# Performance work log

Hardware: AMD Instinct MI355X
Metric: run time of the kernel (lower is better)

## Reference

```python
import jax, jax.numpy as jnp
import numpy as np

D_MODEL = 1024
NUM_HEADS = 16
D_HEAD = D_MODEL // NUM_HEADS
EPS = 1e-06


def setup_inputs() -> dict:
    key = jax.random.key(0)
    ks = jax.random.split(key, 11)
    B, T = 16, 8192
    s = 1.0 / np.sqrt(D_MODEL)
    inp = {
        "query": jax.random.normal(ks[0], (B, 1, D_MODEL), jnp.float32),
        "key": jax.random.normal(ks[1], (B, T, D_MODEL), jnp.float32),
        "value": jax.random.normal(ks[2], (B, T, D_MODEL), jnp.float32),
        "Wq": jax.random.normal(ks[3], (D_MODEL, D_MODEL), jnp.float32) * s,
        "bq": jnp.zeros((D_MODEL,), jnp.float32),
        "Wk": jax.random.normal(ks[4], (D_MODEL, D_MODEL), jnp.float32) * s,
        "bk": jnp.zeros((D_MODEL,), jnp.float32),
        "Wv": jax.random.normal(ks[5], (D_MODEL, D_MODEL), jnp.float32) * s,
        "bv": jnp.zeros((D_MODEL,), jnp.float32),
        "Wo": jax.random.normal(ks[6], (D_MODEL, D_MODEL), jnp.float32) * s,
        "bo": jnp.zeros((D_MODEL,), jnp.float32),
    }
    return inp


def _feature_map(x):
    # ELU + 1 ensures positivity
    return jax.nn.elu(x) + 1.0


def reference(query, key, value, Wq, bq, Wk, bk, Wv, bv, Wo, bo):
    B, T, _ = key.shape
    H, dh = NUM_HEADS, D_HEAD
    # projections (torch Linear: x @ W^T + b)
    Q = (query @ Wq.T + bq).reshape(B, 1, H, dh).transpose(0, 2, 1, 3)  # [B,H,1,dh]
    K = (key @ Wk.T + bk).reshape(B, T, H, dh).transpose(0, 2, 1, 3)    # [B,H,T,dh]
    V = (value @ Wv.T + bv).reshape(B, T, H, dh).transpose(0, 2, 1, 3)  # [B,H,T,dh]
    Q = _feature_map(Q)
    K = _feature_map(K)
    # linear-attention accumulators
    KV = jnp.einsum("bhtd,bhte->bhde", K, V)        # [B,H,dh,dh]
    Z = K.sum(axis=2)                                  # [B,H,dh]
    num = jnp.einsum("bhqd,bhde->bhqe", Q, KV)       # [B,H,1,dh]
    den = jnp.einsum("bhqd,bhd->bhq", Q, Z)[..., None]  # [B,H,1,1]
    out = num / (den + EPS)
    out = out.transpose(0, 2, 1, 3).reshape(B, 1, D_MODEL)
    return out @ Wo.T + bo
```

## Files before the change

kernel.cpp:

```cpp
#include <hip/hip_runtime.h>


typedef __attribute__((ext_vector_type(8))) short  bf16x8;
typedef __attribute__((ext_vector_type(4))) short  bf16x4;
typedef __attribute__((ext_vector_type(4))) float  f32x4;

#define WS_QPHI  0u
#define WS_PRE   65536u
#define WS_S     131072u
#define WS_WKB   1179648u
#define WS_W     3276800u
#define WS_SPART 11665408u
#define WS_NEED  (11665408u + 33554432u)

__device__ __forceinline__ unsigned short f2bf(float f) {
  union { float f; unsigned u; } c; c.f = f;
  unsigned u = c.u;
  return (unsigned short)((u + 0x7fffu + ((u >> 16) & 1u)) >> 16);
}

__device__ __forceinline__ unsigned cvt_pk_bf16(float lo, float hi) {
  unsigned r;
  asm("v_cvt_pk_bf16_f32 %0, %1, %2" : "=v"(r) : "v"(lo), "v"(hi));
  return r;
}

__device__ __forceinline__ uint4 pack_bf16x8(f32x4 x, f32x4 y) {
  uint4 r;
  r.x = cvt_pk_bf16(x[0], x[1]); r.y = cvt_pk_bf16(x[2], x[3]);
  r.z = cvt_pk_bf16(y[0], y[1]); r.w = cvt_pk_bf16(y[2], y[3]);
  return r;
}

__device__ __forceinline__ void gload_lds16(const void* g, void* l) {
  __builtin_amdgcn_global_load_lds((const __attribute__((address_space(1))) void*)g,
                                   (__attribute__((address_space(3))) void*)l, 16, 0, 0);
}

__global__ __launch_bounds__(256)
void k_prep(const float* __restrict__ Wk, unsigned short* __restrict__ Wkb,
            const float* __restrict__ q, const float* __restrict__ Wq,
            const float* __restrict__ bq, float* __restrict__ Qphi) {
  __shared__ float red[4][64];
  const int tid = threadIdx.x;
  if (blockIdx.x < 1024) {
    int i = blockIdx.x * 256 + tid;
    f32x4 v = ((const f32x4*)Wk)[i];
    bf16x4 o;
    o[0] = (short)f2bf(v[0]); o[1] = (short)f2bf(v[1]);
    o[2] = (short)f2bf(v[2]); o[3] = (short)f2bf(v[3]);
    ((bf16x4*)Wkb)[i] = o;
    return;
  }
  const int lin = blockIdx.x - 1024;
  const int h = lin & 15, b = lin >> 4;
  const int d = tid & 63, part = tid >> 6;
  const f32x4* qr = (const f32x4*)(q + b * 1024) + part * 64;
  const f32x4* wr = (const f32x4*)(Wq + (size_t)(h * 64 + d) * 1024) + part * 64;
  float s = 0.f;
  #pragma unroll 8
  for (int i = 0; i < 64; ++i) {
    f32x4 a = qr[i], ww = wr[i];
    s += a[0]*ww[0] + a[1]*ww[1] + a[2]*ww[2] + a[3]*ww[3];
  }
  red[part][d] = s;
  __syncthreads();
  if (part == 0) {
    float t = red[0][d] + red[1][d] + red[2][d] + red[3][d] + bq[h * 64 + d];
    t = t > 0.f ? t + 1.f : __expf(t);
    Qphi[(b * 16 + h) * 64 + d] = t;
  }
}

__global__ __launch_bounds__(512, 4)
void k_kproj(const float* __restrict__ key, const unsigned short* __restrict__ Wkb,
             const float* __restrict__ bk, const float* __restrict__ Qphi,
             float* __restrict__ w) {
  __shared__ __align__(16) unsigned short sA[2][128 * 32];
  __shared__ __align__(16) unsigned short sB[4][256 * 32];

  const int bid  = blockIdx.x + (blockIdx.y << 2);
  const int work = ((bid & 7) << 9) | (bid >> 3);
  const int np   = work & 3;
  const int mb   = work >> 2;
  const int b    = mb >> 6;
  const int mrow = (mb & 63) << 7;
  const int tid  = threadIdx.x;
  const int lane = tid & 63;
  const int wv   = tid >> 6;
  const int wr   = wv >> 2;
  const int wc   = wv & 3;
  const int n0   = np << 8;
  const int h    = (np << 2) | wc;
  const int l15  = lane & 15;
  const int l16  = lane >> 4;

  const int lkx = ((l16 ^ ((l15 >> 1) & 3)) << 3);

  const int ra = tid >> 2, aq = tid & 3;
  const float* Ab = key + ((size_t)((b << 13) + mrow + ra)) * 1024 + aq * 8;
  const int sAoff = ra * 32 + ((aq ^ ((ra >> 1) & 3)) << 3);

  const int bsw = ((lane & 3) ^ ((lane >> 3) & 3)) << 3;
  const unsigned short* Bb = Wkb + ((size_t)(n0 + (wv << 5) + (lane >> 2))) * 1024 + bsw;

  f32x4 acc[4][4];
  #pragma unroll
  for (int i = 0; i < 4; ++i)
    #pragma unroll
    for (int j = 0; j < 4; ++j) acc[i][j] = (f32x4)0.f;

  float qreg[4];
  #pragma unroll
  for (int ni = 0; ni < 4; ++ni)
    qreg[ni] = Qphi[((b << 4) + h) * 64 + ni * 16 + l15];

  f32x4 a0 = *(const f32x4*)(Ab);
  f32x4 a1 = *(const f32x4*)(Ab + 4);
  __builtin_amdgcn_sched_barrier(0);
  gload_lds16(Bb,                  &sB[0][wv * 1024]);
  gload_lds16(Bb + 16 * 1024,      &sB[0][wv * 1024 + 512]);
  gload_lds16(Bb + 32,             &sB[1][wv * 1024]);
  gload_lds16(Bb + 16 * 1024 + 32, &sB[1][wv * 1024 + 512]);
  gload_lds16(Bb + 64,             &sB[2][wv * 1024]);
  gload_lds16(Bb + 16 * 1024 + 64, &sB[2][wv * 1024 + 512]);
  __builtin_amdgcn_sched_barrier(0);
  *(uint4*)&sA[0][sAoff] = pack_bf16x8(a0, a1);
  asm volatile("s_waitcnt vmcnt(2) lgkmcnt(0)" ::: "memory");
  __builtin_amdgcn_s_barrier();
  __builtin_amdgcn_sched_barrier(0);

  bf16x8 bfr[4];
  #pragma unroll
  for (int ni = 0; ni < 4; ++ni)
    bfr[ni] = *(const bf16x8*)&sB[0][((wc << 6) + ni * 16 + l15) * 32 + lkx];

  #pragma unroll 1
  for (int t = 0; t < 32; ++t) {
    if (t < 31) {
      const float* An = Ab + (t + 1) * 32;
      a0 = *(const f32x4*)(An);
      a1 = *(const f32x4*)(An + 4);
    }
    __builtin_amdgcn_sched_barrier(0);
    if (t < 29) {
      const unsigned short* Bn = Bb + (t + 3) * 32;
      const int bn = (t + 3) & 3;
      gload_lds16(Bn,             &sB[bn][wv * 1024]);
      gload_lds16(Bn + 16 * 1024, &sB[bn][wv * 1024 + 512]);
    }
    __builtin_amdgcn_sched_barrier(0);
    {
      const unsigned short* pA = &sA[t & 1][0];
      bf16x8 af[4];
      #pragma unroll
      for (int mi = 0; mi < 4; ++mi)
        af[mi] = *(const bf16x8*)&pA[((wr << 6) + mi * 16 + l15) * 32 + lkx];
      #pragma unroll
      for (int mi = 0; mi < 4; ++mi)
        #pragma unroll
        for (int ni = 0; ni < 4; ++ni)
          acc[mi][ni] = __builtin_amdgcn_mfma_f32_16x16x32_bf16(af[mi], bfr[ni], acc[mi][ni], 0, 0, 0);
    }
    if (t < 31) {
      const unsigned short* pBn = &sB[(t + 1) & 3][0];
      #pragma unroll
      for (int ni = 0; ni < 4; ++ni)
        bfr[ni] = *(const bf16x8*)&pBn[((wc << 6) + ni * 16 + l15) * 32 + lkx];
    }
    if (t < 31)
      *(uint4*)&sA[(t + 1) & 1][sAoff] = pack_bf16x8(a0, a1);
    if (t <= 28)      asm volatile("s_waitcnt vmcnt(2) lgkmcnt(0)" ::: "memory");
    else if (t == 29) asm volatile("s_waitcnt vmcnt(0) lgkmcnt(0)" ::: "memory");
    else if (t == 30) asm volatile("s_waitcnt lgkmcnt(0)" ::: "memory");
    if (t < 31) {
      __builtin_amdgcn_s_barrier();
      __builtin_amdgcn_sched_barrier(0);
    }
  }

  float bias[4];
  #pragma unroll
  for (int ni = 0; ni < 4; ++ni) bias[ni] = bk[n0 + (wc << 6) + ni * 16 + l15];

  #pragma unroll
  for (int mi = 0; mi < 4; ++mi) {
    float wa[4];
    #pragma unroll
    for (int r = 0; r < 4; ++r) {
      float s = 0.f;
      #pragma unroll
      for (int ni = 0; ni < 4; ++ni) {
        float x = acc[mi][ni][r] + bias[ni];
        x = x > 0.f ? x + 1.f : __expf(x);
        s += x * qreg[ni];
      }
      wa[r] = s;
    }
    #pragma unroll
    for (int m = 1; m < 16; m <<= 1)
      #pragma unroll
      for (int r = 0; r < 4; ++r) wa[r] += __shfl_xor(wa[r], m, 64);
    if (l15 == 0) {
      #pragma unroll
      for (int r = 0; r < 4; ++r) {
        int trow = mrow + (wr << 6) + mi * 16 + (l16 << 2) + r;
        w[(((size_t)((b << 4) + h)) << 13) + trow] = wa[r];
      }
    }
  }
}

__global__ __launch_bounds__(256)
void k_sgemm_p(const float* __restrict__ value, const float* __restrict__ w,
               float* __restrict__ Spart) {
  __shared__ float wl[16 * 256];
  const int b = blockIdx.x, tc = blockIdx.y;
  const int t0 = tc << 8;
  const int tid = threadIdx.x;
  for (int i = tid; i < 16 * 256; i += 256)
    wl[i] = w[(((size_t)(b * 16 + (i >> 8))) << 13) + t0 + (i & 255)];
  __syncthreads();
  f32x4 acc[16];
  #pragma unroll
  for (int h = 0; h < 16; ++h) acc[h] = (f32x4)0.f;
  const f32x4* vb  = (const f32x4*)(value + ((size_t)(b << 13) + t0) * 1024) + tid;
  const f32x4* wl4 = (const f32x4*)wl;
  #pragma unroll 1
  for (int tq = 0; tq < 64; ++tq) {
    f32x4 x0 = vb[((tq << 2) + 0) << 8];
    f32x4 x1 = vb[((tq << 2) + 1) << 8];
    f32x4 x2 = vb[((tq << 2) + 2) << 8];
    f32x4 x3 = vb[((tq << 2) + 3) << 8];
    #pragma unroll
    for (int h = 0; h < 16; ++h) {
      f32x4 wv = wl4[(h << 6) + tq];
      acc[h] += x0 * wv[0];
      acc[h] += x1 * wv[1];
      acc[h] += x2 * wv[2];
      acc[h] += x3 * wv[3];
    }
  }
  #pragma unroll
  for (int h = 0; h < 16; ++h) {
    f32x4* op = (f32x4*)(Spart + (((size_t)((b * 32 + tc) * 16 + h)) << 10));
    op[tid] = acc[h];
  }
}

__global__ __launch_bounds__(256)
void k_numden_p(const float* __restrict__ w, const float* __restrict__ Spart,
                const float* __restrict__ Wv, const float* __restrict__ bv,
                float* __restrict__ pre) {
  __shared__ float red[2][4][64];
  const int b = blockIdx.x, h = blockIdx.y;
  const int tid = threadIdx.x, e = tid & 63, part = tid >> 6;
  const float* wb = w + (((size_t)(b * 16 + h)) << 13);
  float dsum = 0.f;
  for (int i = part * 32; i < part * 32 + 32; ++i) dsum += wb[i * 64 + e];
  const f32x4* sp  = (const f32x4*)(Spart + (((size_t)(b * 32 * 16 + h)) << 10));
  const f32x4* wvr = (const f32x4*)(Wv + (size_t)(h * 64 + e) * 1024);
  float ns = 0.f;
  for (int i = part * 64; i < part * 64 + 64; ++i) {
    f32x4 a = (f32x4)0.f;
    #pragma unroll 8
    for (int p = 0; p < 32; ++p) a += sp[p * 4096 + i];
    f32x4 c = wvr[i];
    ns += a[0]*c[0] + a[1]*c[1] + a[2]*c[2] + a[3]*c[3];
  }
  red[0][part][e] = dsum; red[1][part][e] = ns;
  __syncthreads();
  if (part == 0) {
    float d = red[0][0][e] + red[0][1][e] + red[0][2][e] + red[0][3][e];
    float n = red[1][0][e] + red[1][1][e] + red[1][2][e] + red[1][3][e];
    #pragma unroll
    for (int m = 1; m < 64; m <<= 1) d += __shfl_xor(d, m, 64);
    n += d * bv[h * 64 + e];
    pre[b * 1024 + h * 64 + e] = n / (d + 1e-6f);
  }
}

__global__ __launch_bounds__(256)
void k_sgemm(const float* __restrict__ value, const float* __restrict__ w,
             float* __restrict__ S) {
  __shared__ float wl[16 * 256];
  const int b = blockIdx.x, tc = blockIdx.y;
  const int t0 = tc << 8;
  const int tid = threadIdx.x;
  for (int i = tid; i < 16 * 256; i += 256)
    wl[i] = w[(((size_t)(b * 16 + (i >> 8))) << 13) + t0 + (i & 255)];
  __syncthreads();
  f32x4 acc[16];
  #pragma unroll
  for (int h = 0; h < 16; ++h) acc[h] = (f32x4)0.f;
  const f32x4* vb  = (const f32x4*)(value + ((size_t)(b << 13) + t0) * 1024) + tid;
  const f32x4* wl4 = (const f32x4*)wl;
  #pragma unroll 1
  for (int tq = 0; tq < 64; ++tq) {
    f32x4 x0 = vb[((tq << 2) + 0) << 8];
    f32x4 x1 = vb[((tq << 2) + 1) << 8];
    f32x4 x2 = vb[((tq << 2) + 2) << 8];
    f32x4 x3 = vb[((tq << 2) + 3) << 8];
    #pragma unroll
    for (int h = 0; h < 16; ++h) {
      f32x4 wv = wl4[(h << 6) + tq];
      acc[h] += x0 * wv[0]; acc[h] += x1 * wv[1];
      acc[h] += x2 * wv[2]; acc[h] += x3 * wv[3];
    }
  }
  #pragma unroll
  for (int h = 0; h < 16; ++h) {
    float* sp = S + ((b << 4) + h) * 1024 + (tid << 2);
    atomicAdd(sp + 0, acc[h][0]); atomicAdd(sp + 1, acc[h][1]);
    atomicAdd(sp + 2, acc[h][2]); atomicAdd(sp + 3, acc[h][3]);
  }
}

__global__ __launch_bounds__(256)
void k_numden(const float* __restrict__ w, const float* __restrict__ S,
              const float* __restrict__ Wv, const float* __restrict__ bv,
              float* __restrict__ pre) {
  __shared__ float red[2][4][64];
  const int b = blockIdx.x, h = blockIdx.y;
  const int tid = threadIdx.x, e = tid & 63, part = tid >> 6;
  const float* wb = w + (((size_t)(b * 16 + h)) << 13);
  float dsum = 0.f;
  for (int i = part * 32; i < part * 32 + 32; ++i) dsum += wb[i * 64 + e];
  const f32x4* sr  = (const f32x4*)(S + (b * 16 + h) * 1024);
  const f32x4* wvr = (const f32x4*)(Wv + (size_t)(h * 64 + e) * 1024);
  float ns = 0.f;
  for (int i = part * 64; i < part * 64 + 64; ++i) {
    f32x4 a = sr[i], c = wvr[i];
    ns += a[0]*c[0] + a[1]*c[1] + a[2]*c[2] + a[3]*c[3];
  }
  red[0][part][e] = dsum; red[1][part][e] = ns;
  __syncthreads();
  if (part == 0) {
    float d = red[0][0][e] + red[0][1][e] + red[0][2][e] + red[0][3][e];
    float n = red[1][0][e] + red[1][1][e] + red[1][2][e] + red[1][3][e];
    #pragma unroll
    for (int m = 1; m < 64; m <<= 1) d += __shfl_xor(d, m, 64);
    n += d * bv[h * 64 + e];
    pre[b * 1024 + h * 64 + e] = n / (d + 1e-6f);
  }
}

__global__ __launch_bounds__(256)
void k_outproj(const float* __restrict__ pre, const float* __restrict__ Wo,
               const float* __restrict__ bo, float* __restrict__ out) {
  __shared__ float pl[1024];
  const int lin = blockIdx.x;
  const int ch = lin & 7, b = lin >> 3;
  const int tid = threadIdx.x, lane = tid & 63, wv = tid >> 6;
  for (int i = tid; i < 1024; i += 256) pl[i] = pre[b * 1024 + i];
  __syncthreads();
  for (int oi = 0; oi < 32; ++oi) {
    int o = (ch << 7) + (wv << 5) + oi;
    const f32x4* wrow = (const f32x4*)(Wo + (size_t)o * 1024);
    float s = 0.f;
    #pragma unroll
    for (int j = 0; j < 4; ++j) {
      f32x4 v = wrow[lane * 4 + j];
      f32x4 p = *(const f32x4*)&pl[(lane * 4 + j) * 4];
      s += v[0]*p[0] + v[1]*p[1] + v[2]*p[2] + v[3]*p[3];
    }
    #pragma unroll
    for (int m = 1; m < 64; m <<= 1) s += __shfl_xor(s, m, 64);
    if (lane == 0) out[b * 1024 + o] = s + bo[o];
  }
}

extern "C" void kernel_launch(void* const* d_in, const int* in_sizes, int n_in,
                              void* d_out, int out_size, void* d_ws, size_t ws_size,
                              hipStream_t stream) {
  const float* query = (const float*)d_in[0];
  const float* key   = (const float*)d_in[1];
  const float* value = (const float*)d_in[2];
  const float* Wq    = (const float*)d_in[3];
  const float* bq    = (const float*)d_in[4];
  const float* Wk    = (const float*)d_in[5];
  const float* bk    = (const float*)d_in[6];
  const float* Wv    = (const float*)d_in[7];
  const float* bv    = (const float*)d_in[8];
  const float* Wo    = (const float*)d_in[9];
  const float* bo    = (const float*)d_in[10];
  float* out = (float*)d_out;
  char* ws = (char*)d_ws;
  float*          Qphi  = (float*)(ws + WS_QPHI);
  float*          pre   = (float*)(ws + WS_PRE);
  float*          S     = (float*)(ws + WS_S);
  unsigned short* Wkb   = (unsigned short*)(ws + WS_WKB);
  float*          w     = (float*)(ws + WS_W);
  float*          Spart = (float*)(ws + WS_SPART);

  k_prep<<<1280, 256, 0, stream>>>(Wk, Wkb, query, Wq, bq, Qphi);
  k_kproj<<<dim3(4, 1024), 512, 0, stream>>>(key, Wkb, bk, Qphi, w);
  if (ws_size >= (size_t)WS_NEED) {
    k_sgemm_p<<<dim3(16, 32), 256, 0, stream>>>(value, w, Spart);
    k_numden_p<<<dim3(16, 16), 256, 0, stream>>>(w, Spart, Wv, bv, pre);
  } else {
    hipMemsetAsync(S, 0, 16 * 16 * 1024 * sizeof(float), stream);
    k_sgemm<<<dim3(16, 32), 256, 0, stream>>>(value, w, S);
    k_numden<<<dim3(16, 16), 256, 0, stream>>>(w, S, Wv, bv, pre);
  }
  k_outproj<<<128, 256, 0, stream>>>(pre, Wo, bo, out);
}
```

Baseline: 589.1 us.

## Enlarge K-projection GEMM tile to 256 rows per block with 8x4 MFMA per wave

The key-projection GEMM block tile doubles from 128 to 256 rows of keys. Each wave now holds 8x4 accumulators instead of 4x4, and the grid is halved to 2048 blocks. Each Wk tile loaded into LDS is now reused across twice as many rows, cutting B traffic and LDS loads per MFMA. In exchange, accumulator registers and LDS per block go up, launch bounds drop to 2 blocks per CU, and the B-fragment register prefetch across iterations is removed.

```diff
diff --git a/kernel.cpp b/kernel.cpp
--- a/kernel.cpp
+++ b/kernel.cpp
@@ -72,19 +72,19 @@
   }
 }
 
-__global__ __launch_bounds__(512, 4)
+__global__ __launch_bounds__(512, 2)
 void k_kproj(const float* __restrict__ key, const unsigned short* __restrict__ Wkb,
              const float* __restrict__ bk, const float* __restrict__ Qphi,
              float* __restrict__ w) {
-  __shared__ __align__(16) unsigned short sA[2][128 * 32];
+  __shared__ __align__(16) unsigned short sA[2][256 * 32];
   __shared__ __align__(16) unsigned short sB[4][256 * 32];
 
-  const int bid  = blockIdx.x + (blockIdx.y << 2);
-  const int work = ((bid & 7) << 9) | (bid >> 3);
+  const int bid  = blockIdx.x;
+  const int work = ((bid & 7) << 8) | (bid >> 3);
   const int np   = work & 3;
   const int mb   = work >> 2;
-  const int b    = mb >> 6;
-  const int mrow = (mb & 63) << 7;
+  const int b    = mb >> 5;
+  const int mrow = (mb & 31) << 8;
   const int tid  = threadIdx.x;
   const int lane = tid & 63;
   const int wv   = tid >> 6;
@@ -97,16 +97,20 @@
 
   const int lkx = ((l16 ^ ((l15 >> 1) & 3)) << 3);
 
-  const int ra = tid >> 2, aq = tid & 3;
-  const float* Ab = key + ((size_t)((b << 13) + mrow + ra)) * 1024 + aq * 8;
-  const int sAoff = ra * 32 + ((aq ^ ((ra >> 1) & 3)) << 3);
+  const int ar  = tid >> 1;
+  const int ac0 = (tid & 1) << 1;
+  const int aS  = (ar >> 1) & 3;
+  const float* Ab = key + ((size_t)((b << 13) + mrow + ar)) * 1024 + ((tid & 1) << 4);
+  const int aw0 = ar * 32 + ((ac0 ^ aS) << 3);
+  const int aw1 = ar * 32 + (((ac0 | 1) ^ aS) << 3);
 
   const int bsw = ((lane & 3) ^ ((lane >> 3) & 3)) << 3;
-  const unsigned short* Bb = Wkb + ((size_t)(n0 + (wv << 5) + (lane >> 2))) * 1024 + bsw;
-
-  f32x4 acc[4][4];
-  #pragma unroll
-  for (int i = 0; i < 4; ++i)
+  const unsigned short* Bg0 = Wkb + ((size_t)(n0 + (wv << 4) + (lane >> 2))) * 1024 + bsw;
+  const unsigned short* Bg1 = Bg0 + 128 * 1024;
+
+  f32x4 acc[8][4];
+  #pragma unroll
+  for (int i = 0; i < 8; ++i)
     #pragma unroll
     for (int j = 0; j < 4; ++j) acc[i][j] = (f32x4)0.f;
 
@@ -117,23 +121,21 @@
 
   f32x4 a0 = *(const f32x4*)(Ab);
   f32x4 a1 = *(const f32x4*)(Ab + 4);
+  f32x4 a2 = *(const f32x4*)(Ab + 8);
+  f32x4 a3 = *(const f32x4*)(Ab + 12);
   __builtin_amdgcn_sched_barrier(0);
-  gload_lds16(Bb,                  &sB[0][wv * 1024]);
-  gload_lds16(Bb + 16 * 1024,      &sB[0][wv * 1024 + 512]);
-  gload_lds16(Bb + 32,             &sB[1][wv * 1024]);
-  gload_lds16(Bb + 16 * 1024 + 32, &sB[1][wv * 1024 + 512]);
-  gload_lds16(Bb + 64,             &sB[2][wv * 1024]);
-  gload_lds16(Bb + 16 * 1024 + 64, &sB[2][wv * 1024 + 512]);
+  gload_lds16(Bg0,      &sB[0][wv * 512]);
+  gload_lds16(Bg1,      &sB[0][4096 + wv * 512]);
+  gload_lds16(Bg0 + 32, &sB[1][wv * 512]);
+  gload_lds16(Bg1 + 32, &sB[1][4096 + wv * 512]);
+  gload_lds16(Bg0 + 64, &sB[2][wv * 512]);
+  gload_lds16(Bg1 + 64, &sB[2][4096 + wv * 512]);
   __builtin_amdgcn_sched_barrier(0);
-  *(uint4*)&sA[0][sAoff] = pack_bf16x8(a0, a1);
-  asm volatile("s_waitcnt vmcnt(2) lgkmcnt(0)" ::: "memory");
+  *(uint4*)&sA[0][aw0] = pack_bf16x8(a0, a1);
+  *(uint4*)&sA[0][aw1] = pack_bf16x8(a2, a3);
+  asm volatile("s_waitcnt vmcnt(4) lgkmcnt(0)" ::: "memory");
   __builtin_amdgcn_s_barrier();
   __builtin_amdgcn_sched_barrier(0);
-
-  bf16x8 bfr[4];
-  #pragma unroll
-  for (int ni = 0; ni < 4; ++ni)
-    bfr[ni] = *(const bf16x8*)&sB[0][((wc << 6) + ni * 16 + l15) * 32 + lkx];
 
   #pragma unroll 1
   for (int t = 0; t < 32; ++t) {
@@ -141,35 +143,36 @@
       const float* An = Ab + (t + 1) * 32;
       a0 = *(const f32x4*)(An);
       a1 = *(const f32x4*)(An + 4);
+      a2 = *(const f32x4*)(An + 8);
+      a3 = *(const f32x4*)(An + 12);
     }
     __builtin_amdgcn_sched_barrier(0);
     if (t < 29) {
-      const unsigned short* Bn = Bb + (t + 3) * 32;
       const int bn = (t + 3) & 3;
-      gload_lds16(Bn,             &sB[bn][wv * 1024]);
-      gload_lds16(Bn + 16 * 1024, &sB[bn][wv * 1024 + 512]);
+      gload_lds16(Bg0 + (t + 3) * 32, &sB[bn][wv * 512]);
+      gload_lds16(Bg1 + (t + 3) * 32, &sB[bn][4096 + wv * 512]);
     }
     __builtin_amdgcn_sched_barrier(0);
     {
       const unsigned short* pA = &sA[t & 1][0];
-      bf16x8 af[4];
-      #pragma unroll
-      for (int mi = 0; mi < 4; ++mi)
-        af[mi] = *(const bf16x8*)&pA[((wr << 6) + mi * 16 + l15) * 32 + lkx];
-      #pragma unroll
-      for (int mi = 0; mi < 4; ++mi)
+      const unsigned short* pB = &sB[t & 3][0];
+      bf16x8 bfr[4], af[8];
+      #pragma unroll
+      for (int ni = 0; ni < 4; ++ni)
+        bfr[ni] = *(const bf16x8*)&pB[((wc << 6) + ni * 16 + l15) * 32 + lkx];
+      #pragma unroll
+      for (int mi = 0; mi < 8; ++mi)
+        af[mi] = *(const bf16x8*)&pA[((wr << 7) + mi * 16 + l15) * 32 + lkx];
+      #pragma unroll
+      for (int mi = 0; mi < 8; ++mi)
         #pragma unroll
         for (int ni = 0; ni < 4; ++ni)
           acc[mi][ni] = __builtin_amdgcn_mfma_f32_16x16x32_bf16(af[mi], bfr[ni], acc[mi][ni], 0, 0, 0);
     }
     if (t < 31) {
-      const unsigned short* pBn = &sB[(t + 1) & 3][0];
-      #pragma unroll
-      for (int ni = 0; ni < 4; ++ni)
-        bfr[ni] = *(const bf16x8*)&pBn[((wc << 6) + ni * 16 + l15) * 32 + lkx];
-    }
-    if (t < 31)
-      *(uint4*)&sA[(t + 1) & 1][sAoff] = pack_bf16x8(a0, a1);
+      *(uint4*)&sA[(t + 1) & 1][aw0] = pack_bf16x8(a0, a1);
+      *(uint4*)&sA[(t + 1) & 1][aw1] = pack_bf16x8(a2, a3);
+    }
     if (t <= 28)      asm volatile("s_waitcnt vmcnt(2) lgkmcnt(0)" ::: "memory");
     else if (t == 29) asm volatile("s_waitcnt vmcnt(0) lgkmcnt(0)" ::: "memory");
     else if (t == 30) asm volatile("s_waitcnt lgkmcnt(0)" ::: "memory");
@@ -184,7 +187,7 @@
   for (int ni = 0; ni < 4; ++ni) bias[ni] = bk[n0 + (wc << 6) + ni * 16 + l15];
 
   #pragma unroll
-  for (int mi = 0; mi < 4; ++mi) {
+  for (int mi = 0; mi < 8; ++mi) {
     float wa[4];
     #pragma unroll
     for (int r = 0; r < 4; ++r) {
@@ -204,7 +207,7 @@
     if (l15 == 0) {
       #pragma unroll
       for (int r = 0; r < 4; ++r) {
-        int trow = mrow + (wr << 6) + mi * 16 + (l16 << 2) + r;
+        int trow = mrow + (wr << 7) + mi * 16 + (l16 << 2) + r;
         w[(((size_t)((b << 4) + h)) << 13) + trow] = wa[r];
       }
     }
@@ -394,7 +397,7 @@
   float*          Spart = (float*)(ws + WS_SPART);
 
   k_prep<<<1280, 256, 0, stream>>>(Wk, Wkb, query, Wq, bq, Qphi);
-  k_kproj<<<dim3(4, 1024), 512, 0, stream>>>(key, Wkb, bk, Qphi, w);
+  k_kproj<<<2048, 512, 0, stream>>>(key, Wkb, bk, Qphi, w);
   if (ws_size >= (size_t)WS_NEED) {
     k_sgemm_p<<<dim3(16, 32), 256, 0, stream>>>(value, w, Spart);
     k_numden_p<<<dim3(16, 16), 256, 0, stream>>>(w, Spart, Wv, bv, pre);
```

After: 769.6 us. +30.6%, slower.
